# Kernel optimization log

Measured on AMD Instinct MI355X. Metric: run time of the kernel, lower is better.

Reference implementation:

```python
import jax, jax.numpy as jnp
import numpy as np

NH, KD, HD = 8, 32, 32          # n_heads, qk dim, value dim per head
D = NH * HD                     # 256 channels (v.reshape requires d == nh*hd)
SCALE = 0.17677669529663687     # kd ** -0.5


def setup_inputs() -> dict:
    key = jax.random.key(0)
    k1, k2 = jax.random.split(key)
    x = jax.random.normal(k1, (2, D, 64, 64), dtype=jnp.float32)
    # dp[1]: bias-free 1x1 conv D -> NH*(4*KD+HD) = 1280, fan-in scaled
    w_proj = jax.random.normal(k2, (NH * (4 * KD + HD), D), dtype=jnp.float32) * np.float32(1.0 / np.sqrt(D))
    return {"x": x, "w_proj": w_proj}


def reference(x, w_proj):
    b, d, h, w = x.shape
    # dp[0] = Identity; dp[1] = 1x1 conv as a channel matmul
    p = jnp.einsum('bchw,oc->bohw', x, w_proj).reshape(b, NH, 4 * KD + HD, h, w)
    rq = p[:, :, 0 * KD:1 * KD]
    rk = p[:, :, 1 * KD:2 * KD]
    cq = p[:, :, 2 * KD:3 * KD]
    ck = p[:, :, 3 * KD:4 * KD]
    v = p[:, :, 4 * KD:]                      # (b, NH, HD, h, w)
    # row attention over h (independently per column w), softmax over i (dim 2)
    r = jax.nn.softmax(jnp.einsum('bHdiw,bHdjw->bHijw', rq, rk) * SCALE, axis=2)
    # column attention over w (independently per row h), softmax over i (dim 2)
    c = jax.nn.softmax(jnp.einsum('bHdhi,bHdhj->bHihj', cq, ck) * SCALE, axis=2)
    # trilinear combine: out[b,H,d,h,w] = sum_{i,j} r[b,H,i,h,w] * v[b,H,d,i,j] * c[b,H,j,h,w]
    # contract v with c first, then with r (intermediate m is (b,NH,HD,h,h,w))
    m = jnp.einsum('bHdij,bHjhw->bHdihw', v, c)
    out = jnp.einsum('bHihw,bHdihw->bHdhw', r, m).reshape(b, d, h, w)
    # residual: dp[2] = Identity, dp[3] = Identity
    return out + v.reshape(b, d, h, w)
```

## Files before the change

### kernel.cpp

```cpp
#include <hip/hip_runtime.h>
#include <stdint.h>


#define SCALE 0.17677669529663687f
typedef unsigned short ushort_t;
typedef __attribute__((ext_vector_type(8))) short bf16x8;
typedef __attribute__((ext_vector_type(4))) float f32x4;

__device__ __forceinline__ unsigned short f2bf(float f) {
  unsigned int b = __float_as_uint(f);
  b += 0x7fffu + ((b >> 16) & 1u);
  return (unsigned short)(b >> 16);
}
__device__ __forceinline__ float bflo(unsigned int u) { return __uint_as_float(u << 16); }
__device__ __forceinline__ float bfhi(unsigned int u) { return __uint_as_float(u & 0xffff0000u); }
__device__ __forceinline__ unsigned int pk2(float a, float b) {
  return (unsigned int)f2bf(a) | ((unsigned int)f2bf(b) << 16);
}
__device__ __forceinline__ f32x4 mfma16(bf16x8 a, bf16x8 b, f32x4 c) {
  return __builtin_amdgcn_mfma_f32_16x16x32_bf16(a, b, c, 0, 0, 0);
}
__device__ __forceinline__ void gld16(const void* g, void* l) {
  __builtin_amdgcn_global_load_lds(
      (const __attribute__((address_space(1))) unsigned int*)g,
      (__attribute__((address_space(3))) unsigned int*)l, 16, 0, 0);
}

__global__ __launch_bounds__(256) void cvt_w(const float* __restrict__ w,
                                             ushort_t* __restrict__ wbf) {
  const int idx = (blockIdx.x * 256 + threadIdx.x) * 8;
  float4 f0 = *(const float4*)&w[idx];
  float4 f1 = *(const float4*)&w[idx + 4];
  uint4 o; o.x = pk2(f0.x, f0.y); o.y = pk2(f0.z, f0.w);
  o.z = pk2(f1.x, f1.y); o.w = pk2(f1.z, f1.w);
  *(uint4*)&wbf[idx] = o;
}

__global__ __launch_bounds__(256) void xtrans(const float* __restrict__ x,
                                              ushort_t* __restrict__ xt) {
  __shared__ float tile[128][33];
  const int b = blockIdx.z, k0 = blockIdx.y * 32, n0 = blockIdx.x * 128;
  const int t = threadIdx.x;
  const float* xb = x + (size_t)b * 256 * 4096;
#pragma unroll
  for (int rep = 0; rep < 4; rep++) {
    int idx = rep * 256 + t;
    int kk = idx >> 5, nn4 = (idx & 31) * 4;
    float4 f = *(const float4*)&xb[(size_t)(k0 + kk) * 4096 + n0 + nn4];
    tile[nn4 + 0][kk] = f.x; tile[nn4 + 1][kk] = f.y;
    tile[nn4 + 2][kk] = f.z; tile[nn4 + 3][kk] = f.w;
  }
  __syncthreads();
  ushort_t* xo = xt + (size_t)b * 4096 * 256;
#pragma unroll
  for (int rep = 0; rep < 2; rep++) {
    int idx = rep * 256 + t;
    int n = idx >> 2, k8 = (idx & 3) * 8;
    uint4 o;
    o.x = pk2(tile[n][k8 + 0], tile[n][k8 + 1]);
    o.y = pk2(tile[n][k8 + 2], tile[n][k8 + 3]);
    o.z = pk2(tile[n][k8 + 4], tile[n][k8 + 5]);
    o.w = pk2(tile[n][k8 + 6], tile[n][k8 + 7]);
    *(uint4*)&xo[(size_t)(n0 + n) * 256 + k0 + k8] = o;
  }
}

__global__ __launch_bounds__(256, 2) void proj_mfma_v2(const ushort_t* __restrict__ wbf,
                                                       const ushort_t* __restrict__ xt,
                                                       ushort_t* __restrict__ Qr,
                                                       ushort_t* __restrict__ Kr,
                                                       ushort_t* __restrict__ Qc,
                                                       ushort_t* __restrict__ Kc,
                                                       float* __restrict__ P_v) {
  __shared__ ushort_t Af[8 * 64 * 8];
  __shared__ ushort_t Bf[8 * 64 * 8];
  const int b = blockIdx.z, m0 = blockIdx.y * 128, n0 = blockIdx.x * 128;
  const int t = threadIdx.x, wv = t >> 6, l = t & 63;
  const int row = l & 15, quad = l >> 4;
  const int wm = wv >> 1, wn = wv & 1;
  const ushort_t* xb = xt + (size_t)b * 4096 * 256;

  f32x4 acc[4][4];
#pragma unroll
  for (int i = 0; i < 4; i++)
#pragma unroll
    for (int j = 0; j < 4; j++) acc[i][j] = (f32x4){0.f, 0.f, 0.f, 0.f};

  const size_t aoff0 = (size_t)(m0 + (2 * wv + 0) * 16 + row) * 256 + quad * 8;
  const size_t aoff1 = (size_t)(m0 + (2 * wv + 1) * 16 + row) * 256 + quad * 8;
  const size_t boff0 = (size_t)(n0 + (2 * wv + 0) * 16 + row) * 256 + quad * 8;
  const size_t boff1 = (size_t)(n0 + (2 * wv + 1) * 16 + row) * 256 + quad * 8;

  for (int k0 = 0; k0 < 256; k0 += 32) {
    uint4 a0 = *(const uint4*)&wbf[aoff0 + k0];
    uint4 a1 = *(const uint4*)&wbf[aoff1 + k0];
    uint4 b0 = *(const uint4*)&xb[boff0 + k0];
    uint4 b1 = *(const uint4*)&xb[boff1 + k0];
    __syncthreads();
    *(uint4*)&Af[((2 * wv + 0) * 64 + l) * 8] = a0;
    *(uint4*)&Af[((2 * wv + 1) * 64 + l) * 8] = a1;
    *(uint4*)&Bf[((2 * wv + 0) * 64 + l) * 8] = b0;
    *(uint4*)&Bf[((2 * wv + 1) * 64 + l) * 8] = b1;
    __syncthreads();
    bf16x8 af[4], bfr[4];
#pragma unroll
    for (int mf = 0; mf < 4; mf++) af[mf] = *(bf16x8*)&Af[((wm * 4 + mf) * 64 + l) * 8];
#pragma unroll
    for (int nf = 0; nf < 4; nf++) bfr[nf] = *(bf16x8*)&Bf[((wn * 4 + nf) * 64 + l) * 8];
#pragma unroll
    for (int mf = 0; mf < 4; mf++)
#pragma unroll
      for (int nf = 0; nf < 4; nf++)
        acc[mf][nf] = mfma16(af[mf], bfr[nf], acc[mf][nf]);
  }

#pragma unroll
  for (int mf = 0; mf < 4; mf++) {
    int mb = m0 + wm * 64 + mf * 16 + quad * 4;
    int H = mb / 160;
    int rem = mb - H * 160;
    int sec = rem >> 5;
    int d0 = rem & 31;
    int bh = b * 8 + H;
    if (sec < 4) {
      ushort_t* base = (sec == 0) ? Qr : (sec == 1) ? Kr : (sec == 2) ? Qc : Kc;
      base += (size_t)bh * 131072;
#pragma unroll
      for (int nf = 0; nf < 4; nf++) {
        int n = n0 + wn * 64 + nf * 16 + row;
        int orow = (sec < 2) ? ((n & 63) * 64 + (n >> 6)) : n;
        uint2 o;
        o.x = pk2(acc[mf][nf][0], acc[mf][nf][1]);
        o.y = pk2(acc[mf][nf][2], acc[mf][nf][3]);
        *(uint2*)&base[(size_t)orow * 32 + d0] = o;
      }
    } else {
      float* pvb = P_v + ((size_t)bh * 32 + d0) * 4096;
#pragma unroll
      for (int nf = 0; nf < 4; nf++) {
        int n = n0 + wn * 64 + nf * 16 + row;
#pragma unroll
        for (int r = 0; r < 4; r++)
          pvb[(size_t)r * 4096 + n] = acc[mf][nf][r];
      }
    }
  }
}

__global__ __launch_bounds__(256) void scores_mfma(const ushort_t* __restrict__ Qr,
                                                   const ushort_t* __restrict__ Kr,
                                                   const ushort_t* __restrict__ Qc,
                                                   const ushort_t* __restrict__ Kc,
                                                   ushort_t* __restrict__ Rs,
                                                   ushort_t* __restrict__ Cs) {
  const int mode = blockIdx.y;
  const int bh = blockIdx.x >> 4, gq = blockIdx.x & 15;
  const int t = threadIdx.x, wv = t >> 6, l = t & 63;
  const int col = l & 15, quad = l >> 4;
  const int g = gq * 4 + wv;
  const ushort_t* Qb = (mode ? Qc : Qr) + (size_t)bh * 131072 + (size_t)g * 2048;
  const ushort_t* Kb = (mode ? Kc : Kr) + (size_t)bh * 131072 + (size_t)g * 2048;

  bf16x8 aq[4], bk[4];
#pragma unroll
  for (int f = 0; f < 4; f++) {
    aq[f] = *(const bf16x8*)&Qb[(size_t)(f * 16 + col) * 32 + quad * 8];
    bk[f] = *(const bf16x8*)&Kb[(size_t)(f * 16 + col) * 32 + quad * 8];
  }
  f32x4 s[4][4];
#pragma unroll
  for (int i0 = 0; i0 < 4; i0++)
#pragma unroll
    for (int j0 = 0; j0 < 4; j0++)
      s[i0][j0] = mfma16(aq[i0], bk[j0], (f32x4){0.f, 0.f, 0.f, 0.f});

  ushort_t* ob = (mode ? Cs : Rs) + (size_t)bh * 262144;
#pragma unroll
  for (int j0 = 0; j0 < 4; j0++) {
    float sv[16];
#pragma unroll
    for (int i0 = 0; i0 < 4; i0++)
#pragma unroll
      for (int r = 0; r < 4; r++) sv[i0 * 4 + r] = s[i0][j0][r] * SCALE;
    float mx = sv[0];
#pragma unroll
    for (int q = 1; q < 16; q++) mx = fmaxf(mx, sv[q]);
    mx = fmaxf(mx, __shfl_xor(mx, 16));
    mx = fmaxf(mx, __shfl_xor(mx, 32));
    float e[16], sum = 0.f;
#pragma unroll
    for (int q = 0; q < 16; q++) { e[q] = __expf(sv[q] - mx); sum += e[q]; }
    sum += __shfl_xor(sum, 16);
    sum += __shfl_xor(sum, 32);
    const float inv = 1.f / sum;
    const int j = j0 * 16 + col;
#pragma unroll
    for (int i0 = 0; i0 < 4; i0++) {
      uint2 o;
      o.x = pk2(e[i0 * 4 + 0] * inv, e[i0 * 4 + 1] * inv);
      o.y = pk2(e[i0 * 4 + 2] * inv, e[i0 * 4 + 3] * inv);
      size_t addr = mode ? ((size_t)(g * 64 + j) * 64 + i0 * 16 + quad * 4)
                         : ((size_t)(j * 64 + g) * 64 + i0 * 16 + quad * 4);
      *(uint2*)&ob[addr] = o;
    }
  }
}

__global__ __launch_bounds__(256) void vtrans(const float* __restrict__ P_v,
                                              ushort_t* __restrict__ vf) {
  __shared__ float tile[8][64][33];
  const int jc = blockIdx.x;
  const int bh = blockIdx.y;
  const int j0 = jc * 8;
  const float* pvb = P_v + (size_t)bh * 131072;
  const int t = threadIdx.x;
#pragma unroll
  for (int rep = 0; rep < 8; rep++) {
    int idx = rep * 256 + t;
    int d = idx >> 6, i = idx & 63;
    float4 f0 = *(const float4*)&pvb[(size_t)d * 4096 + i * 64 + j0];
    float4 f1 = *(const float4*)&pvb[(size_t)d * 4096 + i * 64 + j0 + 4];
    tile[0][i][d] = f0.x; tile[1][i][d] = f0.y;
    tile[2][i][d] = f0.z; tile[3][i][d] = f0.w;
    tile[4][i][d] = f1.x; tile[5][i][d] = f1.y;
    tile[6][i][d] = f1.z; tile[7][i][d] = f1.w;
  }
  __syncthreads();
  ushort_t* vo = vf + (size_t)bh * 131072;
  const int fid = t >> 6, l = t & 63;
  const int d = (fid & 1) * 16 + (l & 15);
  const int i0 = (fid >> 1) * 32 + (l >> 4) * 8;
#pragma unroll
  for (int rep = 0; rep < 8; rep++) {
    int jl = rep;
    uint4 o;
    o.x = pk2(tile[jl][i0 + 0][d], tile[jl][i0 + 1][d]);
    o.y = pk2(tile[jl][i0 + 2][d], tile[jl][i0 + 3][d]);
    o.z = pk2(tile[jl][i0 + 4][d], tile[jl][i0 + 5][d]);
    o.w = pk2(tile[jl][i0 + 6][d], tile[jl][i0 + 7][d]);
    *(uint4*)&vo[(size_t)(((j0 + jl) * 4 + fid) * 64 + l) * 8] = o;
  }
}

__global__ __launch_bounds__(256, 2) void attn_apply_v4(const float* __restrict__ P_v,
                                                        const ushort_t* __restrict__ rs,
                                                        const ushort_t* __restrict__ cs,
                                                        const ushort_t* __restrict__ vf,
                                                        float* __restrict__ out,
                                                        float* __restrict__ pp1) {
  __shared__ ushort_t buf[2][16384];
  const int bid = blockIdx.x;
  const int jc = bid & 1, pg = (bid >> 1) & 15, bh = bid >> 5;
  const int b = bh >> 3, H = bh & 7;
  const int t = threadIdx.x, wv = t >> 6, l = t & 63;
  const int row = l & 15, quad = l >> 4;
  const int h = pg * 4 + wv;
  const ushort_t* rsl = rs + (size_t)bh * 262144 + (size_t)h * 4096;
  const ushort_t* csl = cs + (size_t)bh * 262144 + (size_t)h * 4096;
  const ushort_t* vchunk = vf + (size_t)bh * 131072 + (size_t)jc * 65536;

  bf16x8 rf[2][4];
#pragma unroll
  for (int nf = 0; nf < 4; nf++)
#pragma unroll
    for (int kc = 0; kc < 2; kc++)
      rf[kc][nf] = *(const bf16x8*)&rsl[(size_t)(nf * 16 + row) * 64 + kc * 32 + quad * 8];

  f32x4 acc[2][4];
#pragma unroll
  for (int i = 0; i < 2; i++)
#pragma unroll
    for (int j = 0; j < 4; j++) acc[i][j] = (f32x4){0.f, 0.f, 0.f, 0.f};

#pragma unroll
  for (int jj = 0; jj < 8; jj++)
    gld16(&vchunk[(size_t)jj * 2048 + wv * 512 + l * 8], &buf[0][jj * 2048 + wv * 512]);
  __syncthreads();

  for (int ph = 0; ph < 4; ph++) {
    const ushort_t* bcur = buf[ph & 1];
    if (ph < 3) {
#pragma unroll
      for (int jj = 0; jj < 8; jj++)
        gld16(&vchunk[(size_t)((ph + 1) * 8 + jj) * 2048 + wv * 512 + l * 8],
              &buf[(ph + 1) & 1][jj * 2048 + wv * 512]);
    }
    float cv[8][4];
#pragma unroll
    for (int nf = 0; nf < 4; nf++) {
      uint4 u = *(const uint4*)&csl[(size_t)(nf * 16 + row) * 64 + jc * 32 + ph * 8];
      cv[0][nf] = bflo(u.x); cv[1][nf] = bfhi(u.x);
      cv[2][nf] = bflo(u.y); cv[3][nf] = bfhi(u.y);
      cv[4][nf] = bflo(u.z); cv[5][nf] = bfhi(u.z);
      cv[6][nf] = bflo(u.w); cv[7][nf] = bfhi(u.w);
    }
#pragma unroll
    for (int jj = 0; jj < 8; jj++) {
      bf16x8 af0[2], af1[2];
#pragma unroll
      for (int mf = 0; mf < 2; mf++) {
        af0[mf] = *(const bf16x8*)&bcur[jj * 2048 + (0 + mf) * 512 + l * 8];
        af1[mf] = *(const bf16x8*)&bcur[jj * 2048 + (2 + mf) * 512 + l * 8];
      }
#pragma unroll
      for (int mf = 0; mf < 2; mf++)
#pragma unroll
        for (int nf = 0; nf < 4; nf++) {
          f32x4 tt = (f32x4){0.f, 0.f, 0.f, 0.f};
          tt = mfma16(af0[mf], rf[0][nf], tt);
          tt = mfma16(af1[mf], rf[1][nf], tt);
          acc[mf][nf] += tt * cv[jj][nf];
        }
    }
    __syncthreads();
  }

  if (jc == 0) {
    const float* pv = P_v + (size_t)bh * 131072 + h * 64;
    float* ob = out + ((size_t)b * 256 + H * 32) * 4096 + h * 64;
#pragma unroll
    for (int mf = 0; mf < 2; mf++)
#pragma unroll
      for (int nf = 0; nf < 4; nf++)
#pragma unroll
        for (int reg = 0; reg < 4; reg++) {
          int d = mf * 16 + quad * 4 + reg;
          int wc = nf * 16 + row;
          ob[(size_t)d * 4096 + wc] = acc[mf][nf][reg] + pv[(size_t)d * 4096 + wc];
        }
  } else {
    float* ob = pp1 + (size_t)bh * 131072 + h * 64;
#pragma unroll
    for (int mf = 0; mf < 2; mf++)
#pragma unroll
      for (int nf = 0; nf < 4; nf++)
#pragma unroll
        for (int reg = 0; reg < 4; reg++) {
          int d = mf * 16 + quad * 4 + reg;
          int wc = nf * 16 + row;
          ob[(size_t)d * 4096 + wc] = acc[mf][nf][reg];
        }
  }
}

__global__ __launch_bounds__(256) void sum_out(float* __restrict__ out,
                                               const float* __restrict__ pp1) {
  const int idx = (blockIdx.x * 256 + threadIdx.x) * 4;
  float4 a = *(const float4*)&out[idx];
  float4 b = *(const float4*)&pp1[idx];
  a.x += b.x; a.y += b.y; a.z += b.z; a.w += b.w;
  *(float4*)&out[idx] = a;
}

extern "C" void kernel_launch(void* const* d_in, const int* in_sizes, int n_in,
                              void* d_out, int out_size, void* d_ws, size_t ws_size,
                              hipStream_t stream) {
  const float* x = (const float*)d_in[0];
  const float* w = (const float*)d_in[1];
  float* out = (float*)d_out;
  float* ws = (float*)d_ws;
  float* P_v = ws;
  ushort_t* Rs  = (ushort_t*)(ws + 2097152);
  ushort_t* Cs  = (ushort_t*)(ws + 4194304);
  ushort_t* Vf  = (ushort_t*)(ws + 6291456);
  ushort_t* Qr  = (ushort_t*)(ws + 7340032);
  ushort_t* Kr  = (ushort_t*)(ws + 8388608);
  ushort_t* Qc  = (ushort_t*)(ws + 9437184);
  ushort_t* Kc  = (ushort_t*)(ws + 10485760);
  ushort_t* Wbf = (ushort_t*)(ws + 11534336);
  ushort_t* Xt  = (ushort_t*)(ws + 11698176);
  float* Pp1 = ws + 12746752;

  cvt_w<<<160, 256, 0, stream>>>(w, Wbf);
  xtrans<<<dim3(32, 8, 2), 256, 0, stream>>>(x, Xt);
  proj_mfma_v2<<<dim3(32, 10, 2), 256, 0, stream>>>(Wbf, Xt, Qr, Kr, Qc, Kc, P_v);
  scores_mfma<<<dim3(256, 2), 256, 0, stream>>>(Qr, Kr, Qc, Kc, Rs, Cs);
  vtrans<<<dim3(8, 16), 256, 0, stream>>>(P_v, Vf);
  attn_apply_v4<<<512, 256, 0, stream>>>(P_v, Rs, Cs, Vf, out, Pp1);
  sum_out<<<2048, 256, 0, stream>>>(out, Pp1);
}
```

Before: 124.9 us.

## Merge prep and mid kernels, pre-swizzle operands into MFMA fragment layout

Merges the weight conversion and x transpose into one prep launch, and the scores and V-transpose kernels into one mid launch, cutting the launch count from seven to five. Both projection operands are now written in MFMA fragment order, so the projection GEMM loads fragments straight from global memory with no LDS staging and no __syncthreads, and its launch bound is raised to four blocks per CU. The cost is less reuse, since each wave reloads its fragments from global/L2 instead of sharing one LDS tile. The merged kernels also reserve the V-transpose LDS tile for every block, including the score blocks that never use it.

```diff
diff --git a/kernel.cpp b/kernel.cpp
--- a/kernel.cpp
+++ b/kernel.cpp
@@ -26,59 +26,71 @@
       (__attribute__((address_space(3))) unsigned int*)l, 16, 0, 0);
 }
 
-__global__ __launch_bounds__(256) void cvt_w(const float* __restrict__ w,
-                                             ushort_t* __restrict__ wbf) {
-  const int idx = (blockIdx.x * 256 + threadIdx.x) * 8;
-  float4 f0 = *(const float4*)&w[idx];
-  float4 f1 = *(const float4*)&w[idx + 4];
-  uint4 o; o.x = pk2(f0.x, f0.y); o.y = pk2(f0.z, f0.w);
-  o.z = pk2(f1.x, f1.y); o.w = pk2(f1.z, f1.w);
-  *(uint4*)&wbf[idx] = o;
-}
-
-__global__ __launch_bounds__(256) void xtrans(const float* __restrict__ x,
-                                              ushort_t* __restrict__ xt) {
-  __shared__ float tile[128][33];
-  const int b = blockIdx.z, k0 = blockIdx.y * 32, n0 = blockIdx.x * 128;
+__global__ __launch_bounds__(256) void prep(const float* __restrict__ x,
+                                            const float* __restrict__ w,
+                                            ushort_t* __restrict__ xtf,
+                                            ushort_t* __restrict__ wf) {
+  const int bid = blockIdx.x;
   const int t = threadIdx.x;
-  const float* xb = x + (size_t)b * 256 * 4096;
-#pragma unroll
-  for (int rep = 0; rep < 4; rep++) {
-    int idx = rep * 256 + t;
-    int kk = idx >> 5, nn4 = (idx & 31) * 4;
-    float4 f = *(const float4*)&xb[(size_t)(k0 + kk) * 4096 + n0 + nn4];
-    tile[nn4 + 0][kk] = f.x; tile[nn4 + 1][kk] = f.y;
-    tile[nn4 + 2][kk] = f.z; tile[nn4 + 3][kk] = f.w;
-  }
-  __syncthreads();
-  ushort_t* xo = xt + (size_t)b * 4096 * 256;
-#pragma unroll
-  for (int rep = 0; rep < 2; rep++) {
-    int idx = rep * 256 + t;
-    int n = idx >> 2, k8 = (idx & 3) * 8;
-    uint4 o;
-    o.x = pk2(tile[n][k8 + 0], tile[n][k8 + 1]);
-    o.y = pk2(tile[n][k8 + 2], tile[n][k8 + 3]);
-    o.z = pk2(tile[n][k8 + 4], tile[n][k8 + 5]);
-    o.w = pk2(tile[n][k8 + 6], tile[n][k8 + 7]);
-    *(uint4*)&xo[(size_t)(n0 + n) * 256 + k0 + k8] = o;
-  }
-}
-
-__global__ __launch_bounds__(256, 2) void proj_mfma_v2(const ushort_t* __restrict__ wbf,
-                                                       const ushort_t* __restrict__ xt,
+  if (bid < 512) {
+    __shared__ float tile[128][33];
+    const int b = bid >> 8, rem = bid & 255;
+    const int kc = rem >> 5;
+    const int n0 = (rem & 31) * 128;
+    const float* xb = x + (size_t)b * 256 * 4096;
+#pragma unroll
+    for (int rep = 0; rep < 4; rep++) {
+      int idx = rep * 256 + t;
+      int kk = idx >> 5, nn4 = (idx & 31) * 4;
+      float4 f = *(const float4*)&xb[(size_t)(kc * 32 + kk) * 4096 + n0 + nn4];
+      tile[nn4 + 0][kk] = f.x; tile[nn4 + 1][kk] = f.y;
+      tile[nn4 + 2][kk] = f.z; tile[nn4 + 3][kk] = f.w;
+    }
+    __syncthreads();
+    ushort_t* xo = xtf + (size_t)b * 1048576;
+#pragma unroll
+    for (int rep = 0; rep < 2; rep++) {
+      int idx = rep * 256 + t;
+      int n = idx >> 2, k8 = (idx & 3) * 8;
+      uint4 o;
+      o.x = pk2(tile[n][k8 + 0], tile[n][k8 + 1]);
+      o.y = pk2(tile[n][k8 + 2], tile[n][k8 + 3]);
+      o.z = pk2(tile[n][k8 + 4], tile[n][k8 + 5]);
+      o.w = pk2(tile[n][k8 + 6], tile[n][k8 + 7]);
+      int nt = (n0 + n) >> 4;
+      int lane = ((n0 + n) & 15) + ((k8 >> 3) << 4);
+      *(uint4*)&xo[(size_t)((nt * 8 + kc) * 64 + lane) * 8] = o;
+    }
+  } else {
+    const int mt = bid - 512;
+    const int wv = t >> 6, l = t & 63;
+#pragma unroll
+    for (int s = 0; s < 2; s++) {
+      int kc = wv + s * 4;
+      const float* src = &w[(size_t)(mt * 16 + (l & 15)) * 256 + kc * 32 + (l >> 4) * 8];
+      float4 f0 = *(const float4*)&src[0];
+      float4 f1 = *(const float4*)&src[4];
+      uint4 o;
+      o.x = pk2(f0.x, f0.y); o.y = pk2(f0.z, f0.w);
+      o.z = pk2(f1.x, f1.y); o.w = pk2(f1.z, f1.w);
+      *(uint4*)&wf[(size_t)((mt * 8 + kc) * 64 + l) * 8] = o;
+    }
+  }
+}
+
+__global__ __launch_bounds__(256, 4) void proj_mfma_v3(const ushort_t* __restrict__ wf,
+                                                       const ushort_t* __restrict__ xtf,
                                                        ushort_t* __restrict__ Qr,
                                                        ushort_t* __restrict__ Kr,
                                                        ushort_t* __restrict__ Qc,
                                                        ushort_t* __restrict__ Kc,
                                                        float* __restrict__ P_v) {
-  __shared__ ushort_t Af[8 * 64 * 8];
-  __shared__ ushort_t Bf[8 * 64 * 8];
-  const int b = blockIdx.z, m0 = blockIdx.y * 128, n0 = blockIdx.x * 128;
+  const int b = blockIdx.z, by = blockIdx.y, bx = blockIdx.x;
+  const int m0 = by * 128, n0 = bx * 128;
   const int t = threadIdx.x, wv = t >> 6, l = t & 63;
   const int row = l & 15, quad = l >> 4;
   const int wm = wv >> 1, wn = wv & 1;
-  const ushort_t* xb = xt + (size_t)b * 4096 * 256;
+  const ushort_t* xb = xtf + (size_t)b * 1048576;
 
   f32x4 acc[4][4];
 #pragma unroll
@@ -86,27 +98,17 @@
 #pragma unroll
     for (int j = 0; j < 4; j++) acc[i][j] = (f32x4){0.f, 0.f, 0.f, 0.f};
 
-  const size_t aoff0 = (size_t)(m0 + (2 * wv + 0) * 16 + row) * 256 + quad * 8;
-  const size_t aoff1 = (size_t)(m0 + (2 * wv + 1) * 16 + row) * 256 + quad * 8;
-  const size_t boff0 = (size_t)(n0 + (2 * wv + 0) * 16 + row) * 256 + quad * 8;
-  const size_t boff1 = (size_t)(n0 + (2 * wv + 1) * 16 + row) * 256 + quad * 8;
-
-  for (int k0 = 0; k0 < 256; k0 += 32) {
-    uint4 a0 = *(const uint4*)&wbf[aoff0 + k0];
-    uint4 a1 = *(const uint4*)&wbf[aoff1 + k0];
-    uint4 b0 = *(const uint4*)&xb[boff0 + k0];
-    uint4 b1 = *(const uint4*)&xb[boff1 + k0];
-    __syncthreads();
-    *(uint4*)&Af[((2 * wv + 0) * 64 + l) * 8] = a0;
-    *(uint4*)&Af[((2 * wv + 1) * 64 + l) * 8] = a1;
-    *(uint4*)&Bf[((2 * wv + 0) * 64 + l) * 8] = b0;
-    *(uint4*)&Bf[((2 * wv + 1) * 64 + l) * 8] = b1;
-    __syncthreads();
+  const size_t abase = (size_t)(by * 8 + wm * 4) * 4096 + l * 8;
+  const size_t bbase = (size_t)(bx * 8 + wn * 4) * 4096 + l * 8;
+
+  for (int kc = 0; kc < 8; kc++) {
     bf16x8 af[4], bfr[4];
 #pragma unroll
-    for (int mf = 0; mf < 4; mf++) af[mf] = *(bf16x8*)&Af[((wm * 4 + mf) * 64 + l) * 8];
-#pragma unroll
-    for (int nf = 0; nf < 4; nf++) bfr[nf] = *(bf16x8*)&Bf[((wn * 4 + nf) * 64 + l) * 8];
+    for (int mf = 0; mf < 4; mf++)
+      af[mf] = *(const bf16x8*)&wf[abase + mf * 4096 + kc * 512];
+#pragma unroll
+    for (int nf = 0; nf < 4; nf++)
+      bfr[nf] = *(const bf16x8*)&xb[bbase + nf * 4096 + kc * 512];
 #pragma unroll
     for (int mf = 0; mf < 4; mf++)
 #pragma unroll
@@ -147,98 +149,100 @@
   }
 }
 
-__global__ __launch_bounds__(256) void scores_mfma(const ushort_t* __restrict__ Qr,
-                                                   const ushort_t* __restrict__ Kr,
-                                                   const ushort_t* __restrict__ Qc,
-                                                   const ushort_t* __restrict__ Kc,
-                                                   ushort_t* __restrict__ Rs,
-                                                   ushort_t* __restrict__ Cs) {
-  const int mode = blockIdx.y;
-  const int bh = blockIdx.x >> 4, gq = blockIdx.x & 15;
+__global__ __launch_bounds__(256) void mid(const ushort_t* __restrict__ Qr,
+                                           const ushort_t* __restrict__ Kr,
+                                           const ushort_t* __restrict__ Qc,
+                                           const ushort_t* __restrict__ Kc,
+                                           ushort_t* __restrict__ Rs,
+                                           ushort_t* __restrict__ Cs,
+                                           const float* __restrict__ P_v,
+                                           ushort_t* __restrict__ vf) {
+  __shared__ float tile[8][64][33];
+  const int bid = blockIdx.x;
   const int t = threadIdx.x, wv = t >> 6, l = t & 63;
-  const int col = l & 15, quad = l >> 4;
-  const int g = gq * 4 + wv;
-  const ushort_t* Qb = (mode ? Qc : Qr) + (size_t)bh * 131072 + (size_t)g * 2048;
-  const ushort_t* Kb = (mode ? Kc : Kr) + (size_t)bh * 131072 + (size_t)g * 2048;
-
-  bf16x8 aq[4], bk[4];
-#pragma unroll
-  for (int f = 0; f < 4; f++) {
-    aq[f] = *(const bf16x8*)&Qb[(size_t)(f * 16 + col) * 32 + quad * 8];
-    bk[f] = *(const bf16x8*)&Kb[(size_t)(f * 16 + col) * 32 + quad * 8];
-  }
-  f32x4 s[4][4];
-#pragma unroll
-  for (int i0 = 0; i0 < 4; i0++)
-#pragma unroll
-    for (int j0 = 0; j0 < 4; j0++)
-      s[i0][j0] = mfma16(aq[i0], bk[j0], (f32x4){0.f, 0.f, 0.f, 0.f});
-
-  ushort_t* ob = (mode ? Cs : Rs) + (size_t)bh * 262144;
-#pragma unroll
-  for (int j0 = 0; j0 < 4; j0++) {
-    float sv[16];
+  if (bid < 512) {
+    const int mode = bid >> 8;
+    const int idx = bid & 255;
+    const int bh = idx >> 4, gq = idx & 15;
+    const int col = l & 15, quad = l >> 4;
+    const int g = gq * 4 + wv;
+    const ushort_t* Qb = (mode ? Qc : Qr) + (size_t)bh * 131072 + (size_t)g * 2048;
+    const ushort_t* Kb = (mode ? Kc : Kr) + (size_t)bh * 131072 + (size_t)g * 2048;
+
+    bf16x8 aq[4], bk[4];
+#pragma unroll
+    for (int f = 0; f < 4; f++) {
+      aq[f] = *(const bf16x8*)&Qb[(size_t)(f * 16 + col) * 32 + quad * 8];
+      bk[f] = *(const bf16x8*)&Kb[(size_t)(f * 16 + col) * 32 + quad * 8];
+    }
+    f32x4 s[4][4];
 #pragma unroll
     for (int i0 = 0; i0 < 4; i0++)
 #pragma unroll
-      for (int r = 0; r < 4; r++) sv[i0 * 4 + r] = s[i0][j0][r] * SCALE;
-    float mx = sv[0];
-#pragma unroll
-    for (int q = 1; q < 16; q++) mx = fmaxf(mx, sv[q]);
-    mx = fmaxf(mx, __shfl_xor(mx, 16));
-    mx = fmaxf(mx, __shfl_xor(mx, 32));
-    float e[16], sum = 0.f;
-#pragma unroll
-    for (int q = 0; q < 16; q++) { e[q] = __expf(sv[q] - mx); sum += e[q]; }
-    sum += __shfl_xor(sum, 16);
-    sum += __shfl_xor(sum, 32);
-    const float inv = 1.f / sum;
-    const int j = j0 * 16 + col;
-#pragma unroll
-    for (int i0 = 0; i0 < 4; i0++) {
-      uint2 o;
-      o.x = pk2(e[i0 * 4 + 0] * inv, e[i0 * 4 + 1] * inv);
-      o.y = pk2(e[i0 * 4 + 2] * inv, e[i0 * 4 + 3] * inv);
-      size_t addr = mode ? ((size_t)(g * 64 + j) * 64 + i0 * 16 + quad * 4)
-                         : ((size_t)(j * 64 + g) * 64 + i0 * 16 + quad * 4);
-      *(uint2*)&ob[addr] = o;
-    }
-  }
-}
-
-__global__ __launch_bounds__(256) void vtrans(const float* __restrict__ P_v,
-                                              ushort_t* __restrict__ vf) {
-  __shared__ float tile[8][64][33];
-  const int jc = blockIdx.x;
-  const int bh = blockIdx.y;
-  const int j0 = jc * 8;
-  const float* pvb = P_v + (size_t)bh * 131072;
-  const int t = threadIdx.x;
-#pragma unroll
-  for (int rep = 0; rep < 8; rep++) {
-    int idx = rep * 256 + t;
-    int d = idx >> 6, i = idx & 63;
-    float4 f0 = *(const float4*)&pvb[(size_t)d * 4096 + i * 64 + j0];
-    float4 f1 = *(const float4*)&pvb[(size_t)d * 4096 + i * 64 + j0 + 4];
-    tile[0][i][d] = f0.x; tile[1][i][d] = f0.y;
-    tile[2][i][d] = f0.z; tile[3][i][d] = f0.w;
-    tile[4][i][d] = f1.x; tile[5][i][d] = f1.y;
-    tile[6][i][d] = f1.z; tile[7][i][d] = f1.w;
-  }
-  __syncthreads();
-  ushort_t* vo = vf + (size_t)bh * 131072;
-  const int fid = t >> 6, l = t & 63;
-  const int d = (fid & 1) * 16 + (l & 15);
-  const int i0 = (fid >> 1) * 32 + (l >> 4) * 8;
-#pragma unroll
-  for (int rep = 0; rep < 8; rep++) {
-    int jl = rep;
-    uint4 o;
-    o.x = pk2(tile[jl][i0 + 0][d], tile[jl][i0 + 1][d]);
-    o.y = pk2(tile[jl][i0 + 2][d], tile[jl][i0 + 3][d]);
-    o.z = pk2(tile[jl][i0 + 4][d], tile[jl][i0 + 5][d]);
-    o.w = pk2(tile[jl][i0 + 6][d], tile[jl][i0 + 7][d]);
-    *(uint4*)&vo[(size_t)(((j0 + jl) * 4 + fid) * 64 + l) * 8] = o;
+      for (int j0 = 0; j0 < 4; j0++)
+        s[i0][j0] = mfma16(aq[i0], bk[j0], (f32x4){0.f, 0.f, 0.f, 0.f});
+
+    ushort_t* ob = (mode ? Cs : Rs) + (size_t)bh * 262144;
+#pragma unroll
+    for (int j0 = 0; j0 < 4; j0++) {
+      float sv[16];
+#pragma unroll
+      for (int i0 = 0; i0 < 4; i0++)
+#pragma unroll
+        for (int r = 0; r < 4; r++) sv[i0 * 4 + r] = s[i0][j0][r] * SCALE;
+      float mx = sv[0];
+#pragma unroll
+      for (int q = 1; q < 16; q++) mx = fmaxf(mx, sv[q]);
+      mx = fmaxf(mx, __shfl_xor(mx, 16));
+      mx = fmaxf(mx, __shfl_xor(mx, 32));
+      float e[16], sum = 0.f;
+#pragma unroll
+      for (int q = 0; q < 16; q++) { e[q] = __expf(sv[q] - mx); sum += e[q]; }
+      sum += __shfl_xor(sum, 16);
+      sum += __shfl_xor(sum, 32);
+      const float inv = 1.f / sum;
+      const int j = j0 * 16 + col;
+#pragma unroll
+      for (int i0 = 0; i0 < 4; i0++) {
+        uint2 o;
+        o.x = pk2(e[i0 * 4 + 0] * inv, e[i0 * 4 + 1] * inv);
+        o.y = pk2(e[i0 * 4 + 2] * inv, e[i0 * 4 + 3] * inv);
+        size_t addr = mode ? ((size_t)(g * 64 + j) * 64 + i0 * 16 + quad * 4)
+                           : ((size_t)(j * 64 + g) * 64 + i0 * 16 + quad * 4);
+        *(uint2*)&ob[addr] = o;
+      }
+    }
+  } else {
+    const int vid = bid - 512;
+    const int jc = vid & 7, bh = vid >> 3;
+    const int j0 = jc * 8;
+    const float* pvb = P_v + (size_t)bh * 131072;
+#pragma unroll
+    for (int rep = 0; rep < 8; rep++) {
+      int idx = rep * 256 + t;
+      int d = idx >> 6, i = idx & 63;
+      float4 f0 = *(const float4*)&pvb[(size_t)d * 4096 + i * 64 + j0];
+      float4 f1 = *(const float4*)&pvb[(size_t)d * 4096 + i * 64 + j0 + 4];
+      tile[0][i][d] = f0.x; tile[1][i][d] = f0.y;
+      tile[2][i][d] = f0.z; tile[3][i][d] = f0.w;
+      tile[4][i][d] = f1.x; tile[5][i][d] = f1.y;
+      tile[6][i][d] = f1.z; tile[7][i][d] = f1.w;
+    }
+    __syncthreads();
+    ushort_t* vo = vf + (size_t)bh * 131072;
+    const int fid = t >> 6;
+    const int d = (fid & 1) * 16 + (l & 15);
+    const int i0 = (fid >> 1) * 32 + (l >> 4) * 8;
+#pragma unroll
+    for (int rep = 0; rep < 8; rep++) {
+      int jl = rep;
+      uint4 o;
+      o.x = pk2(tile[jl][i0 + 0][d], tile[jl][i0 + 1][d]);
+      o.y = pk2(tile[jl][i0 + 2][d], tile[jl][i0 + 3][d]);
+      o.z = pk2(tile[jl][i0 + 4][d], tile[jl][i0 + 5][d]);
+      o.w = pk2(tile[jl][i0 + 6][d], tile[jl][i0 + 7][d]);
+      *(uint4*)&vo[(size_t)(((j0 + jl) * 4 + fid) * 64 + l) * 8] = o;
+    }
   }
 }
 
@@ -367,15 +371,13 @@
   ushort_t* Kr  = (ushort_t*)(ws + 8388608);
   ushort_t* Qc  = (ushort_t*)(ws + 9437184);
   ushort_t* Kc  = (ushort_t*)(ws + 10485760);
-  ushort_t* Wbf = (ushort_t*)(ws + 11534336);
-  ushort_t* Xt  = (ushort_t*)(ws + 11698176);
+  ushort_t* Wf  = (ushort_t*)(ws + 11534336);
+  ushort_t* Xtf = (ushort_t*)(ws + 11698176);
   float* Pp1 = ws + 12746752;
 
-  cvt_w<<<160, 256, 0, stream>>>(w, Wbf);
-  xtrans<<<dim3(32, 8, 2), 256, 0, stream>>>(x, Xt);
-  proj_mfma_v2<<<dim3(32, 10, 2), 256, 0, stream>>>(Wbf, Xt, Qr, Kr, Qc, Kc, P_v);
-  scores_mfma<<<dim3(256, 2), 256, 0, stream>>>(Qr, Kr, Qc, Kc, Rs, Cs);
-  vtrans<<<dim3(8, 16), 256, 0, stream>>>(P_v, Vf);
+  prep<<<592, 256, 0, stream>>>(x, w, Xtf, Wf);
+  proj_mfma_v3<<<dim3(32, 10, 2), 256, 0, stream>>>(Wf, Xtf, Qr, Kr, Qc, Kc, P_v);
+  mid<<<640, 256, 0, stream>>>(Qr, Kr, Qc, Kc, Rs, Cs, P_v, Vf);
   attn_apply_v4<<<512, 256, 0, stream>>>(P_v, Rs, Cs, Vf, out, Pp1);
   sum_out<<<2048, 256, 0, stream>>>(out, Pp1);
 }
```

New measurement: 120.1 us. -3.8%, faster.
